# Kernel optimization log

Measured on AMD Instinct MI355X. Metric: run time of the kernel, lower is better.

Reference implementation:

```python
import jax, jax.numpy as jnp
import numpy as np

N_NODES = 50000
N_EDGES = 500000
IN_CH = 128
OUT_CH = 64
HEADS = 4


def setup_inputs() -> dict:
    key = jax.random.key(0)
    ks = jax.random.split(key, 9)
    x = jax.random.normal(ks[0], (N_NODES, IN_CH), dtype=jnp.float32)
    edge_index = jax.random.randint(ks[1], (2, N_EDGES), 0, N_NODES, dtype=jnp.int64)
    edge_weights = jax.random.uniform(ks[2], (N_EDGES, 1), dtype=jnp.float32)
    # xavier-uniform params, stored as [in, out] so y = x @ W
    def xavier(k, shape):
        fan_in, fan_out = shape
        lim = float(np.sqrt(6.0 / (fan_in + fan_out)))
        return jax.random.uniform(k, shape, minval=-lim, maxval=lim, dtype=jnp.float32)
    Wq = xavier(ks[3], (IN_CH, OUT_CH * HEADS))
    Wk = xavier(ks[4], (IN_CH, OUT_CH * HEADS))
    Wv = xavier(ks[5], (IN_CH, OUT_CH * HEADS))
    We = xavier(ks[6], (1, HEADS))
    Wout = xavier(ks[7], (OUT_CH * HEADS, OUT_CH))
    b_out = jnp.zeros((OUT_CH,), dtype=jnp.float32)
    return {"x": x, "edge_index": edge_index, "edge_weights": edge_weights,
            "Wq": Wq, "Wk": Wk, "Wv": Wv, "We": We, "Wout": Wout, "b_out": b_out}


def reference(x, edge_index, edge_weights, Wq, Wk, Wv, We, Wout, b_out):
    num_nodes = x.shape[0]
    src = edge_index[0]
    tgt = edge_index[1]
    x_src = x[src]                                    # [E, in]
    x_tgt = x[tgt]                                    # [E, in]
    q = (x_tgt @ Wq).reshape(-1, HEADS, OUT_CH)       # [E, H, C]
    k = (x_src @ Wk).reshape(-1, HEADS, OUT_CH)
    v = (x_src @ Wv).reshape(-1, HEADS, OUT_CH)
    attn = jnp.sum(q * k, axis=-1) / jnp.sqrt(jnp.float32(OUT_CH))  # [E, H]
    attn = attn + edge_weights @ We                   # [E, H]
    attn = jax.nn.leaky_relu(attn, negative_slope=0.2)
    attn = jax.nn.softmax(attn, axis=0)               # global softmax over edges (as in source)
    weighted_v = attn[..., None] * v                  # [E, H, C]
    out = jax.ops.segment_sum(weighted_v, tgt, num_segments=num_nodes)  # [N, H, C]
    out = out.reshape(num_nodes, HEADS * OUT_CH) @ Wout + b_out         # [N, out]
    if x.shape == out.shape:
        out = out + x
    return out
```

## Files before the change

kernel.cpp:

```cpp
#include <hip/hip_runtime.h>
#include <hip/hip_bf16.h>
#include <hip/hip_fp16.h>

#define N_NODES 50000
#define N_EDGES 500000
#define IN_CH   128
#define D       256
#define UDIM    512
#define OUT_CH  64
#define HEADS   4
#define NC      49

typedef _Float16 half8 __attribute__((ext_vector_type(8)));
typedef _Float16 half2_t __attribute__((ext_vector_type(2)));
typedef float   floatx4 __attribute__((ext_vector_type(4)));

__global__ __launch_bounds__(256) void prep_kernel(const float* __restrict__ x,
                                                   __half* __restrict__ x16,
                                                   int* __restrict__ cnt,
                                                   double* __restrict__ S) {
    int i = blockIdx.x * 256 + threadIdx.x;
    if (i < N_NODES) cnt[i] = 0;
    if (i < HEADS) S[i] = 0.0;
    int k = i * 4;
    if (k < N_NODES * IN_CH) {
        float4 v = *(const float4*)(x + k);
        union { __half2 h[2]; uint2 u; } pk;
        pk.h[0] = __floats2half2_rn(v.x, v.y);
        pk.h[1] = __floats2half2_rn(v.z, v.w);
        *(uint2*)(x16 + k) = pk.u;
    }
}

__global__ __launch_bounds__(128) void wbuild_kernel(const float* __restrict__ Wq,
                                                     const float* __restrict__ Wk,
                                                     const float* __restrict__ Wv,
                                                     const float* __restrict__ Wout,
                                                     __half* __restrict__ M16t,
                                                     __half* __restrict__ Zc16t) {
    __shared__ float buf[64];
    const int tid = threadIdx.x;
    if (blockIdx.x < 512) {
        const int r = blockIdx.x;
        const int h = r >> 7, j = r & 127;
        if (tid < 64) buf[tid] = Wk[(size_t)j * D + h * 64 + tid];
        __syncthreads();
        const float4* qr = (const float4*)(Wq + (size_t)tid * D + h * 64);
        float s = 0.f;
        #pragma unroll
        for (int c4 = 0; c4 < 16; ++c4) {
            float4 q = qr[c4];
            s += q.x * buf[c4 * 4] + q.y * buf[c4 * 4 + 1]
               + q.z * buf[c4 * 4 + 2] + q.w * buf[c4 * 4 + 3];
        }
        M16t[(size_t)r * IN_CH + tid] = __float2half(s);
    } else {
        const int r = blockIdx.x - 512;
        const int h = r >> 7, i = r & 127;
        if (tid < 64) buf[tid] = Wv[(size_t)i * D + h * 64 + tid];
        __syncthreads();
        if (tid < 64) {
            float s = 0.f;
            #pragma unroll 8
            for (int j = 0; j < 64; ++j)
                s += buf[j] * Wout[(size_t)(h * 64 + j) * OUT_CH + tid];
            Zc16t[(size_t)tid * UDIM + r] = __float2half(s);
        }
    }
}

__global__ __launch_bounds__(256) void gemm_u_mfma_kernel(const __half* __restrict__ x16,
                                                          const __half* __restrict__ M16t,
                                                          __half* __restrict__ u16) {
    __shared__ __half Ax[128][136];
    __shared__ __half Bm[128][136];
    const int m0 = blockIdx.x * 128;
    const int colbase = blockIdx.y * 128;
    const int tid = threadIdx.x;

    {
        const int r = tid >> 1, part = tid & 1;
        uint4 va[8];
        if (m0 + r < N_NODES) {
            const uint4* src = (const uint4*)(x16 + (size_t)(m0 + r) * IN_CH + part * 64);
            #pragma unroll
            for (int q = 0; q < 8; ++q) va[q] = src[q];
        } else {
            #pragma unroll
            for (int q = 0; q < 8; ++q) va[q] = make_uint4(0u, 0u, 0u, 0u);
        }
        uint4* da = (uint4*)&Ax[r][part * 64];
        #pragma unroll
        for (int q = 0; q < 8; ++q) da[q] = va[q];
        const uint4* sb = (const uint4*)(M16t + (size_t)(colbase + r) * IN_CH + part * 64);
        uint4* db = (uint4*)&Bm[r][part * 64];
        #pragma unroll
        for (int q = 0; q < 8; ++q) db[q] = sb[q];
    }
    __syncthreads();

    const int w = tid >> 6, lane = tid & 63;
    const int mrow = lane & 15, quad = lane >> 4;

    half8 a[2][4];
    #pragma unroll
    for (int mt = 0; mt < 2; ++mt)
        #pragma unroll
        for (int ks = 0; ks < 4; ++ks)
            a[mt][ks] = *(const half8*)&Ax[w * 32 + mt * 16 + mrow][ks * 32 + quad * 8];

    floatx4 acc[2][8];
    #pragma unroll
    for (int mt = 0; mt < 2; ++mt)
        #pragma unroll
        for (int nt = 0; nt < 8; ++nt)
            acc[mt][nt] = (floatx4){0.f, 0.f, 0.f, 0.f};

    #pragma unroll
    for (int nt = 0; nt < 8; ++nt) {
        #pragma unroll
        for (int ks = 0; ks < 4; ++ks) {
            half8 b = *(const half8*)&Bm[nt * 16 + mrow][ks * 32 + quad * 8];
            acc[0][nt] = __builtin_amdgcn_mfma_f32_16x16x32_f16(a[0][ks], b, acc[0][nt], 0, 0, 0);
            acc[1][nt] = __builtin_amdgcn_mfma_f32_16x16x32_f16(a[1][ks], b, acc[1][nt], 0, 0, 0);
        }
    }
    __syncthreads();
    #pragma unroll
    for (int mt = 0; mt < 2; ++mt)
        #pragma unroll
        for (int nt = 0; nt < 8; ++nt)
            #pragma unroll
            for (int r = 0; r < 4; ++r)
                Ax[w * 32 + mt * 16 + quad * 4 + r][nt * 16 + mrow] = __float2half(acc[mt][nt][r]);
    __syncthreads();
    {
        const int r = tid >> 1, part = tid & 1;
        if (m0 + r < N_NODES) {
            const uint4* s4 = (const uint4*)&Ax[r][part * 64];
            uint4* d4 = (uint4*)(u16 + (size_t)(m0 + r) * UDIM + colbase + part * 64);
            #pragma unroll
            for (int q = 0; q < 8; ++q) d4[q] = s4[q];
        }
    }
}

__global__ __launch_bounds__(256) void hist_kernel(const int* __restrict__ ei,
                                                   int* __restrict__ cnt) {
    int e = blockIdx.x * 256 + threadIdx.x;
    if (e < N_EDGES) atomicAdd(&cnt[ei[N_EDGES + e]], 1);
}

__global__ __launch_bounds__(256) void scan_reduce_kernel(const int* __restrict__ cnt,
                                                          int* __restrict__ csum) {
    const int b = blockIdx.x, tid = threadIdx.x;
    const int lane = tid & 63, wid = tid >> 6;
    int s = 0;
    int idx0 = b * 1024 + tid * 4;
    #pragma unroll
    for (int i = 0; i < 4; ++i) {
        int idx = idx0 + i;
        if (idx < N_NODES) s += cnt[idx];
    }
    #pragma unroll
    for (int m = 1; m < 64; m <<= 1) s += __shfl_xor(s, m, 64);
    __shared__ int w[4];
    if (lane == 0) w[wid] = s;
    __syncthreads();
    if (tid == 0) csum[b] = w[0] + w[1] + w[2] + w[3];
}

__global__ __launch_bounds__(64) void scan_top_kernel(int* __restrict__ csum) {
    int lane = threadIdx.x;
    int v = (lane < NC) ? csum[lane] : 0;
    int x = v;
    #pragma unroll
    for (int d = 1; d < 64; d <<= 1) {
        int y = __shfl_up(x, d, 64);
        if (lane >= d) x += y;
    }
    if (lane < NC) csum[lane] = x - v;
}

__global__ __launch_bounds__(256) void scan_chunks_kernel(int* __restrict__ cnt,
                                                          const int* __restrict__ csum,
                                                          int* __restrict__ rp) {
    const int b = blockIdx.x, tid = threadIdx.x;
    const int lane = tid & 63, wid = tid >> 6;
    __shared__ int wsum[4];
    int v[4];
    const int idx0 = b * 1024 + tid * 4;
    #pragma unroll
    for (int i = 0; i < 4; ++i) {
        int idx = idx0 + i;
        v[i] = (idx < N_NODES) ? cnt[idx] : 0;
    }
    int tsum = v[0] + v[1] + v[2] + v[3];
    int x = tsum;
    #pragma unroll
    for (int d = 1; d < 64; d <<= 1) {
        int y = __shfl_up(x, d, 64);
        if (lane >= d) x += y;
    }
    if (lane == 63) wsum[wid] = x;
    __syncthreads();
    int woff = 0;
    for (int w = 0; w < wid; ++w) woff += wsum[w];
    int excl = csum[b] + woff + x - tsum;
    #pragma unroll
    for (int i = 0; i < 4; ++i) {
        int idx = idx0 + i;
        if (idx < N_NODES) { rp[idx] = excl; cnt[idx] = excl; }
        excl += v[i];
    }
}

__global__ __launch_bounds__(256) void scatter_kernel(const int* __restrict__ ei,
                                                      const float* __restrict__ ew,
                                                      int* __restrict__ cnt,
                                                      int2* __restrict__ payload) {
    int e = blockIdx.x * 256 + threadIdx.x;
    if (e >= N_EDGES) return;
    int s = ei[e], t = ei[N_EDGES + e];
    int pos = atomicAdd(&cnt[t], 1);
    payload[pos] = make_int2(s, __float_as_int(ew[e]));
}

__global__ __launch_bounds__(256) void edge_fused_kernel(const __half* __restrict__ u16,
                                                         const __half* __restrict__ x16,
                                                         const int* __restrict__ rp,
                                                         const int* __restrict__ cnt,
                                                         const int2* __restrict__ payload,
                                                         const float* __restrict__ We,
                                                         __half* __restrict__ y16,
                                                         double* __restrict__ S) {
    const int tid = threadIdx.x;
    const int l16 = tid & 15;
    const int h = l16 >> 2;
    const int q = l16 & 3;
    const int node = blockIdx.x * 16 + (tid >> 4);
    const float wev = We[h];

    uint4 ur[4];
    {
        const uint4* ub = (const uint4*)(u16 + (size_t)node * UDIM + h * 128 + q * 32);
        ur[0] = ub[0]; ur[1] = ub[1]; ur[2] = ub[2]; ur[3] = ub[3];
    }
    const half2_t* uh = (const half2_t*)ur;

    half2_t yacc[16];
    #pragma unroll
    for (int t = 0; t < 16; ++t) yacc[t] = (half2_t){(_Float16)0.f, (_Float16)0.f};

    float sacc = 0.f;
    const int start = rp[node];
    const int end = cnt[node];
    int2 pl = make_int2(0, 0);
    uint4 xr[4];
    if (start < end) {
        pl = payload[start];
        const uint4* xb = (const uint4*)(x16 + (size_t)pl.x * IN_CH + q * 32);
        xr[0] = xb[0]; xr[1] = xb[1]; xr[2] = xb[2]; xr[3] = xb[3];
    }
    for (int e = start; e < end; ++e) {
        int2 pln = pl;
        uint4 xrn[4] = {xr[0], xr[1], xr[2], xr[3]};
        if (e + 1 < end) {
            pln = payload[e + 1];
            const uint4* xb = (const uint4*)(x16 + (size_t)pln.x * IN_CH + q * 32);
            xrn[0] = xb[0]; xrn[1] = xb[1]; xrn[2] = xb[2]; xrn[3] = xb[3];
        }
        const half2_t* xh = (const half2_t*)xr;
        float dot = 0.f;
        #pragma unroll
        for (int t = 0; t < 16; ++t)
            dot = __builtin_amdgcn_fdot2(uh[t], xh[t], dot, false);
        dot += __shfl_xor(dot, 1, 16);
        dot += __shfl_xor(dot, 2, 16);
        float l = dot * 0.125f + __int_as_float(pl.y) * wev;
        l = fmaxf(l, 0.2f * l);
        float p = __expf(l);
        if (q == 0) sacc += p;
        half2_t p2 = (half2_t){(_Float16)p, (_Float16)p};
        #pragma unroll
        for (int t = 0; t < 16; ++t)
            yacc[t] = p2 * xh[t] + yacc[t];
        pl = pln;
        xr[0] = xrn[0]; xr[1] = xrn[1]; xr[2] = xrn[2]; xr[3] = xrn[3];
    }
    {
        uint4* yo = (uint4*)(y16 + (size_t)node * UDIM + h * 128 + q * 32);
        const uint4* ys = (const uint4*)yacc;
        yo[0] = ys[0]; yo[1] = ys[1]; yo[2] = ys[2]; yo[3] = ys[3];
    }
    __shared__ float sblk[4];
    if (tid < 4) sblk[tid] = 0.f;
    __syncthreads();
    if (q == 0) atomicAdd(&sblk[h], sacc);
    __syncthreads();
    if (tid < 4) atomicAdd(&S[tid], (double)sblk[tid]);
}

__global__ __launch_bounds__(256) void gemm_out_mfma_kernel(const __half* __restrict__ y16,
                                                            const __half* __restrict__ Zc16t,
                                                            const double* __restrict__ S,
                                                            const float* __restrict__ b_out,
                                                            float* __restrict__ out) {
    __shared__ __half Ay[128][136];
    __shared__ __half Bz[64][136];
    __shared__ float invs_s[4];
    const int m0 = blockIdx.x * 128;
    const int tid = threadIdx.x;
    if (tid < 4) invs_s[tid] = (float)(1.0 / S[tid]);

    const int w = tid >> 6, lane = tid & 63;
    const int mrow = lane & 15, quad = lane >> 4;

    floatx4 result[2][4];
    #pragma unroll
    for (int mt = 0; mt < 2; ++mt)
        #pragma unroll
        for (int nt = 0; nt < 4; ++nt)
            result[mt][nt] = (floatx4){0.f, 0.f, 0.f, 0.f};

    for (int h = 0; h < HEADS; ++h) {
        {
            const int r = tid >> 1, part = tid & 1;
            uint4 va[8];
            if (m0 + r < N_NODES) {
                const uint4* src = (const uint4*)(y16 + (size_t)(m0 + r) * UDIM + h * 128 + part * 64);
                #pragma unroll
                for (int qq = 0; qq < 8; ++qq) va[qq] = src[qq];
            } else {
                #pragma unroll
                for (int qq = 0; qq < 8; ++qq) va[qq] = make_uint4(0u, 0u, 0u, 0u);
            }
            uint4* da = (uint4*)&Ay[r][part * 64];
            #pragma unroll
            for (int qq = 0; qq < 8; ++qq) da[qq] = va[qq];
        }
        {
            const int r = tid >> 2, part = tid & 3;
            const uint4* sb = (const uint4*)(Zc16t + (size_t)r * UDIM + h * 128 + part * 32);
            uint4* db = (uint4*)&Bz[r][part * 32];
            #pragma unroll
            for (int qq = 0; qq < 4; ++qq) db[qq] = sb[qq];
        }
        __syncthreads();

        half8 a[2][4];
        #pragma unroll
        for (int mt = 0; mt < 2; ++mt)
            #pragma unroll
            for (int ks = 0; ks < 4; ++ks)
                a[mt][ks] = *(const half8*)&Ay[w * 32 + mt * 16 + mrow][ks * 32 + quad * 8];

        floatx4 acc[2][4];
        #pragma unroll
        for (int mt = 0; mt < 2; ++mt)
            #pragma unroll
            for (int nt = 0; nt < 4; ++nt)
                acc[mt][nt] = (floatx4){0.f, 0.f, 0.f, 0.f};

        #pragma unroll
        for (int nt = 0; nt < 4; ++nt) {
            #pragma unroll
            for (int ks = 0; ks < 4; ++ks) {
                half8 b = *(const half8*)&Bz[nt * 16 + mrow][ks * 32 + quad * 8];
                acc[0][nt] = __builtin_amdgcn_mfma_f32_16x16x32_f16(a[0][ks], b, acc[0][nt], 0, 0, 0);
                acc[1][nt] = __builtin_amdgcn_mfma_f32_16x16x32_f16(a[1][ks], b, acc[1][nt], 0, 0, 0);
            }
        }
        const float inv = invs_s[h];
        #pragma unroll
        for (int mt = 0; mt < 2; ++mt)
            #pragma unroll
            for (int nt = 0; nt < 4; ++nt) {
                result[mt][nt][0] += inv * acc[mt][nt][0];
                result[mt][nt][1] += inv * acc[mt][nt][1];
                result[mt][nt][2] += inv * acc[mt][nt][2];
                result[mt][nt][3] += inv * acc[mt][nt][3];
            }
        __syncthreads();
    }
    float bcol[4];
    #pragma unroll
    for (int nt = 0; nt < 4; ++nt) bcol[nt] = b_out[nt * 16 + mrow];
    #pragma unroll
    for (int mt = 0; mt < 2; ++mt) {
        #pragma unroll
        for (int r = 0; r < 4; ++r) {
            int row = m0 + w * 32 + mt * 16 + quad * 4 + r;
            if (row < N_NODES) {
                float* dst = out + (size_t)row * OUT_CH;
                #pragma unroll
                for (int nt = 0; nt < 4; ++nt)
                    dst[nt * 16 + mrow] = result[mt][nt][r] + bcol[nt];
            }
        }
    }
}

extern "C" void kernel_launch(void* const* d_in, const int* in_sizes, int n_in,
                              void* d_out, int out_size, void* d_ws, size_t ws_size,
                              hipStream_t stream) {
    const float* x     = (const float*)d_in[0];
    const int*   ei    = (const int*)d_in[1];
    const float* ew    = (const float*)d_in[2];
    const float* Wq    = (const float*)d_in[3];
    const float* Wk    = (const float*)d_in[4];
    const float* Wv    = (const float*)d_in[5];
    const float* We    = (const float*)d_in[6];
    const float* Wout  = (const float*)d_in[7];
    const float* b_out = (const float*)d_in[8];
    float* out = (float*)d_out;

    __half* u16   = (__half*)d_ws;
    __half* y16   = u16 + (size_t)N_NODES * UDIM;
    __half* x16   = y16 + (size_t)N_NODES * UDIM;
    double* S     = (double*)(x16 + (size_t)N_NODES * IN_CH);
    __half* M16t  = (__half*)(S + HEADS);
    __half* Zc16t = M16t + UDIM * IN_CH;
    int*    rp    = (int*)(Zc16t + OUT_CH * UDIM);
    int*    cnt   = rp + N_NODES;
    int*    csum  = cnt + N_NODES;
    int2*   payload = (int2*)(csum + 64);

    prep_kernel<<<(N_NODES * IN_CH / 4 + 255) / 256, 256, 0, stream>>>(x, x16, cnt, S);
    wbuild_kernel<<<1024, 128, 0, stream>>>(Wq, Wk, Wv, Wout, M16t, Zc16t);
    gemm_u_mfma_kernel<<<dim3((N_NODES + 127) / 128, 4), 256, 0, stream>>>(x16, M16t, u16);
    hist_kernel<<<(N_EDGES + 255) / 256, 256, 0, stream>>>(ei, cnt);
    scan_reduce_kernel<<<NC, 256, 0, stream>>>(cnt, csum);
    scan_top_kernel<<<1, 64, 0, stream>>>(csum);
    scan_chunks_kernel<<<NC, 256, 0, stream>>>(cnt, csum, rp);
    scatter_kernel<<<(N_EDGES + 255) / 256, 256, 0, stream>>>(ei, ew, cnt, payload);
    edge_fused_kernel<<<N_NODES / 16, 256, 0, stream>>>(u16, x16, rp, cnt, payload, We, y16, S);
    gemm_out_mfma_kernel<<<(N_NODES + 127) / 128, 256, 0, stream>>>(y16, Zc16t, S, b_out, out);
}
```

Before: 272.5 us.

## Fuse per-node u projection GEMM into edge kernel via LDS

Removes the standalone gemm_u kernel and computes each block's 16 nodes' 512-wide u vectors with MFMA at the start of the edge kernel, staging them in shared memory. This eliminates writing and re-reading the 50000x512 fp16 u buffer through global memory plus one launch. In exchange each edge block reloads the full M16t matrix from global or cache, the MFMA tiles are only 16 rows so B reuse is low, and LDS use rises, which may reduce occupancy of the latency-bound gather loop.

```diff
diff --git a/kernel.cpp b/kernel.cpp
--- a/kernel.cpp
+++ b/kernel.cpp
@@ -69,82 +69,6 @@
     }
 }
 
-__global__ __launch_bounds__(256) void gemm_u_mfma_kernel(const __half* __restrict__ x16,
-                                                          const __half* __restrict__ M16t,
-                                                          __half* __restrict__ u16) {
-    __shared__ __half Ax[128][136];
-    __shared__ __half Bm[128][136];
-    const int m0 = blockIdx.x * 128;
-    const int colbase = blockIdx.y * 128;
-    const int tid = threadIdx.x;
-
-    {
-        const int r = tid >> 1, part = tid & 1;
-        uint4 va[8];
-        if (m0 + r < N_NODES) {
-            const uint4* src = (const uint4*)(x16 + (size_t)(m0 + r) * IN_CH + part * 64);
-            #pragma unroll
-            for (int q = 0; q < 8; ++q) va[q] = src[q];
-        } else {
-            #pragma unroll
-            for (int q = 0; q < 8; ++q) va[q] = make_uint4(0u, 0u, 0u, 0u);
-        }
-        uint4* da = (uint4*)&Ax[r][part * 64];
-        #pragma unroll
-        for (int q = 0; q < 8; ++q) da[q] = va[q];
-        const uint4* sb = (const uint4*)(M16t + (size_t)(colbase + r) * IN_CH + part * 64);
-        uint4* db = (uint4*)&Bm[r][part * 64];
-        #pragma unroll
-        for (int q = 0; q < 8; ++q) db[q] = sb[q];
-    }
-    __syncthreads();
-
-    const int w = tid >> 6, lane = tid & 63;
-    const int mrow = lane & 15, quad = lane >> 4;
-
-    half8 a[2][4];
-    #pragma unroll
-    for (int mt = 0; mt < 2; ++mt)
-        #pragma unroll
-        for (int ks = 0; ks < 4; ++ks)
-            a[mt][ks] = *(const half8*)&Ax[w * 32 + mt * 16 + mrow][ks * 32 + quad * 8];
-
-    floatx4 acc[2][8];
-    #pragma unroll
-    for (int mt = 0; mt < 2; ++mt)
-        #pragma unroll
-        for (int nt = 0; nt < 8; ++nt)
-            acc[mt][nt] = (floatx4){0.f, 0.f, 0.f, 0.f};
-
-    #pragma unroll
-    for (int nt = 0; nt < 8; ++nt) {
-        #pragma unroll
-        for (int ks = 0; ks < 4; ++ks) {
-            half8 b = *(const half8*)&Bm[nt * 16 + mrow][ks * 32 + quad * 8];
-            acc[0][nt] = __builtin_amdgcn_mfma_f32_16x16x32_f16(a[0][ks], b, acc[0][nt], 0, 0, 0);
-            acc[1][nt] = __builtin_amdgcn_mfma_f32_16x16x32_f16(a[1][ks], b, acc[1][nt], 0, 0, 0);
-        }
-    }
-    __syncthreads();
-    #pragma unroll
-    for (int mt = 0; mt < 2; ++mt)
-        #pragma unroll
-        for (int nt = 0; nt < 8; ++nt)
-            #pragma unroll
-            for (int r = 0; r < 4; ++r)
-                Ax[w * 32 + mt * 16 + quad * 4 + r][nt * 16 + mrow] = __float2half(acc[mt][nt][r]);
-    __syncthreads();
-    {
-        const int r = tid >> 1, part = tid & 1;
-        if (m0 + r < N_NODES) {
-            const uint4* s4 = (const uint4*)&Ax[r][part * 64];
-            uint4* d4 = (uint4*)(u16 + (size_t)(m0 + r) * UDIM + colbase + part * 64);
-            #pragma unroll
-            for (int q = 0; q < 8; ++q) d4[q] = s4[q];
-        }
-    }
-}
-
 __global__ __launch_bounds__(256) void hist_kernel(const int* __restrict__ ei,
                                                    int* __restrict__ cnt) {
     int e = blockIdx.x * 256 + threadIdx.x;
@@ -226,27 +150,53 @@
     payload[pos] = make_int2(s, __float_as_int(ew[e]));
 }
 
-__global__ __launch_bounds__(256) void edge_fused_kernel(const __half* __restrict__ u16,
-                                                         const __half* __restrict__ x16,
+__global__ __launch_bounds__(256) void edge_fused_kernel(const __half* __restrict__ x16,
+                                                         const __half* __restrict__ M16t,
                                                          const int* __restrict__ rp,
                                                          const int* __restrict__ cnt,
                                                          const int2* __restrict__ payload,
                                                          const float* __restrict__ We,
                                                          __half* __restrict__ y16,
                                                          double* __restrict__ S) {
+    __shared__ __half u_lds[16][520];
     const int tid = threadIdx.x;
+    const int nodebase = blockIdx.x * 16;
+
+    {
+        const int w = tid >> 6, lane = tid & 63;
+        const int mrow = lane & 15, quad = lane >> 4;
+        half8 a[4];
+        #pragma unroll
+        for (int ks = 0; ks < 4; ++ks)
+            a[ks] = *(const half8*)(x16 + (size_t)(nodebase + mrow) * IN_CH + ks * 32 + quad * 8);
+        #pragma unroll
+        for (int nt8 = 0; nt8 < 8; ++nt8) {
+            const int nt = w * 8 + nt8;
+            floatx4 acc = (floatx4){0.f, 0.f, 0.f, 0.f};
+            #pragma unroll
+            for (int ks = 0; ks < 4; ++ks) {
+                half8 b = *(const half8*)(M16t + (size_t)(nt * 16 + mrow) * IN_CH + ks * 32 + quad * 8);
+                acc = __builtin_amdgcn_mfma_f32_16x16x32_f16(a[ks], b, acc, 0, 0, 0);
+            }
+            #pragma unroll
+            for (int r = 0; r < 4; ++r)
+                u_lds[quad * 4 + r][nt * 16 + mrow] = __float2half(acc[r]);
+        }
+    }
+    __syncthreads();
+
     const int l16 = tid & 15;
     const int h = l16 >> 2;
     const int q = l16 & 3;
-    const int node = blockIdx.x * 16 + (tid >> 4);
+    const int node = nodebase + (tid >> 4);
     const float wev = We[h];
 
-    uint4 ur[4];
+    uint4 ur4[4];
     {
-        const uint4* ub = (const uint4*)(u16 + (size_t)node * UDIM + h * 128 + q * 32);
-        ur[0] = ub[0]; ur[1] = ub[1]; ur[2] = ub[2]; ur[3] = ub[3];
-    }
-    const half2_t* uh = (const half2_t*)ur;
+        const uint4* ub = (const uint4*)&u_lds[tid >> 4][h * 128 + q * 32];
+        ur4[0] = ub[0]; ur4[1] = ub[1]; ur4[2] = ub[2]; ur4[3] = ub[3];
+    }
+    const half2_t* uh = (const half2_t*)ur4;
 
     half2_t yacc[16];
     #pragma unroll
@@ -415,8 +365,7 @@
     const float* b_out = (const float*)d_in[8];
     float* out = (float*)d_out;
 
-    __half* u16   = (__half*)d_ws;
-    __half* y16   = u16 + (size_t)N_NODES * UDIM;
+    __half* y16   = (__half*)d_ws;
     __half* x16   = y16 + (size_t)N_NODES * UDIM;
     double* S     = (double*)(x16 + (size_t)N_NODES * IN_CH);
     __half* M16t  = (__half*)(S + HEADS);
@@ -428,12 +377,11 @@
 
     prep_kernel<<<(N_NODES * IN_CH / 4 + 255) / 256, 256, 0, stream>>>(x, x16, cnt, S);
     wbuild_kernel<<<1024, 128, 0, stream>>>(Wq, Wk, Wv, Wout, M16t, Zc16t);
-    gemm_u_mfma_kernel<<<dim3((N_NODES + 127) / 128, 4), 256, 0, stream>>>(x16, M16t, u16);
     hist_kernel<<<(N_EDGES + 255) / 256, 256, 0, stream>>>(ei, cnt);
     scan_reduce_kernel<<<NC, 256, 0, stream>>>(cnt, csum);
     scan_top_kernel<<<1, 64, 0, stream>>>(csum);
     scan_chunks_kernel<<<NC, 256, 0, stream>>>(cnt, csum, rp);
     scatter_kernel<<<(N_EDGES + 255) / 256, 256, 0, stream>>>(ei, ew, cnt, payload);
-    edge_fused_kernel<<<N_NODES / 16, 256, 0, stream>>>(u16, x16, rp, cnt, payload, We, y16, S);
+    edge_fused_kernel<<<N_NODES / 16, 256, 0, stream>>>(x16, M16t, rp, cnt, payload, We, y16, S);
     gemm_out_mfma_kernel<<<(N_NODES + 127) / 128, 256, 0, stream>>>(y16, Zc16t, S, b_out, out);
 }
```

Result: slower. 443.6 us (+62.8%).

## Sort nodes by in-degree bucket to balance edge kernel warps

Applied to the files above, without the earlier changes.

Adds a counting sort of nodes by in-degree (histogram, scan, scatter into a permutation), and the fused edge kernel now processes nodes in that order. Nodes that share a wavefront get similar degrees, so lanes spend less time idle while waiting for the longest edge loop. The cost is three extra small kernel launches and an indirection through perm. Adjacent wavefronts also no longer touch contiguous node rows, which hurts locality of the u16 and y16 accesses.

```diff
diff --git a/kernel.cpp b/kernel.cpp
--- a/kernel.cpp
+++ b/kernel.cpp
@@ -10,6 +10,7 @@
 #define OUT_CH  64
 #define HEADS   4
 #define NC      49
+#define DBUCK   128
 
 typedef _Float16 half8 __attribute__((ext_vector_type(8)));
 typedef _Float16 half2_t __attribute__((ext_vector_type(2)));
@@ -18,9 +19,11 @@
 __global__ __launch_bounds__(256) void prep_kernel(const float* __restrict__ x,
                                                    __half* __restrict__ x16,
                                                    int* __restrict__ cnt,
+                                                   int* __restrict__ dcnt,
                                                    double* __restrict__ S) {
     int i = blockIdx.x * 256 + threadIdx.x;
     if (i < N_NODES) cnt[i] = 0;
+    if (i < DBUCK) dcnt[i] = 0;
     if (i < HEADS) S[i] = 0.0;
     int k = i * 4;
     if (k < N_NODES * IN_CH) {
@@ -151,6 +154,38 @@
     if (e < N_EDGES) atomicAdd(&cnt[ei[N_EDGES + e]], 1);
 }
 
+__global__ __launch_bounds__(256) void deghist_kernel(const int* __restrict__ cnt,
+                                                      int* __restrict__ dcnt) {
+    int i = blockIdx.x * 256 + threadIdx.x;
+    if (i < N_NODES) atomicAdd(&dcnt[min(cnt[i], DBUCK - 1)], 1);
+}
+
+__global__ __launch_bounds__(128) void degscan_kernel(int* __restrict__ dcnt) {
+    const int tid = threadIdx.x, lane = tid & 63, wid = tid >> 6;
+    int v = dcnt[tid];
+    int x = v;
+    #pragma unroll
+    for (int d = 1; d < 64; d <<= 1) {
+        int y = __shfl_up(x, d, 64);
+        if (lane >= d) x += y;
+    }
+    __shared__ int w0;
+    if (wid == 0 && lane == 63) w0 = x;
+    __syncthreads();
+    dcnt[tid] = x - v + (wid ? w0 : 0);
+}
+
+__global__ __launch_bounds__(256) void degscatter_kernel(const int* __restrict__ cnt,
+                                                         int* __restrict__ dcnt,
+                                                         int* __restrict__ perm) {
+    int i = blockIdx.x * 256 + threadIdx.x;
+    if (i < N_NODES) {
+        int b = min(cnt[i], DBUCK - 1);
+        int pos = atomicAdd(&dcnt[b], 1);
+        perm[pos] = i;
+    }
+}
+
 __global__ __launch_bounds__(256) void scan_reduce_kernel(const int* __restrict__ cnt,
                                                           int* __restrict__ csum) {
     const int b = blockIdx.x, tid = threadIdx.x;
@@ -228,6 +263,7 @@
 
 __global__ __launch_bounds__(256) void edge_fused_kernel(const __half* __restrict__ u16,
                                                          const __half* __restrict__ x16,
+                                                         const int* __restrict__ perm,
                                                          const int* __restrict__ rp,
                                                          const int* __restrict__ cnt,
                                                          const int2* __restrict__ payload,
@@ -238,15 +274,15 @@
     const int l16 = tid & 15;
     const int h = l16 >> 2;
     const int q = l16 & 3;
-    const int node = blockIdx.x * 16 + (tid >> 4);
+    const int node = perm[blockIdx.x * 16 + (tid >> 4)];
     const float wev = We[h];
 
-    uint4 ur[4];
+    uint4 ur4[4];
     {
         const uint4* ub = (const uint4*)(u16 + (size_t)node * UDIM + h * 128 + q * 32);
-        ur[0] = ub[0]; ur[1] = ub[1]; ur[2] = ub[2]; ur[3] = ub[3];
-    }
-    const half2_t* uh = (const half2_t*)ur;
+        ur4[0] = ub[0]; ur4[1] = ub[1]; ur4[2] = ub[2]; ur4[3] = ub[3];
+    }
+    const half2_t* uh = (const half2_t*)ur4;
 
     half2_t yacc[16];
     #pragma unroll
@@ -424,16 +460,21 @@
     int*    rp    = (int*)(Zc16t + OUT_CH * UDIM);
     int*    cnt   = rp + N_NODES;
     int*    csum  = cnt + N_NODES;
-    int2*   payload = (int2*)(csum + 64);
-
-    prep_kernel<<<(N_NODES * IN_CH / 4 + 255) / 256, 256, 0, stream>>>(x, x16, cnt, S);
+    int*    dcnt  = csum + 64;
+    int*    perm  = dcnt + DBUCK;
+    int2*   payload = (int2*)(perm + N_NODES);
+
+    prep_kernel<<<(N_NODES * IN_CH / 4 + 255) / 256, 256, 0, stream>>>(x, x16, cnt, dcnt, S);
     wbuild_kernel<<<1024, 128, 0, stream>>>(Wq, Wk, Wv, Wout, M16t, Zc16t);
     gemm_u_mfma_kernel<<<dim3((N_NODES + 127) / 128, 4), 256, 0, stream>>>(x16, M16t, u16);
     hist_kernel<<<(N_EDGES + 255) / 256, 256, 0, stream>>>(ei, cnt);
+    deghist_kernel<<<(N_NODES + 255) / 256, 256, 0, stream>>>(cnt, dcnt);
+    degscan_kernel<<<1, 128, 0, stream>>>(dcnt);
+    degscatter_kernel<<<(N_NODES + 255) / 256, 256, 0, stream>>>(cnt, dcnt, perm);
     scan_reduce_kernel<<<NC, 256, 0, stream>>>(cnt, csum);
     scan_top_kernel<<<1, 64, 0, stream>>>(csum);
     scan_chunks_kernel<<<NC, 256, 0, stream>>>(cnt, csum, rp);
     scatter_kernel<<<(N_EDGES + 255) / 256, 256, 0, stream>>>(ei, ew, cnt, payload);
-    edge_fused_kernel<<<N_NODES / 16, 256, 0, stream>>>(u16, x16, rp, cnt, payload, We, y16, S);
+    edge_fused_kernel<<<N_NODES / 16, 256, 0, stream>>>(u16, x16, perm, rp, cnt, payload, We, y16, S);
     gemm_out_mfma_kernel<<<(N_NODES + 127) / 128, 256, 0, stream>>>(y16, Zc16t, S, b_out, out);
 }
```

Result: slower. 589.7 us (+116.4%).

## Merge prep, histogram, weight build and scan stages into fewer launches; stage payload in LDS

Applied to the files above, without the earlier changes.

Cuts the launch count from ten to six: x->fp16 conversion, edge histogram and both weight-product builds now share one kernel, the chunk-sum reduction rides along with the u GEMM, and the top-level scan is computed redundantly inside each scan_chunks block. The cnt zeroing moves to a memset. The edge kernel also stages each block's contiguous payload span into shared memory, falling back to global memory past a 1024-entry cap. The aim is to remove launch gaps and small serial kernels, at the cost of mixed-role blocks and extra LDS use in the edge kernel.

```diff
diff --git a/kernel.cpp b/kernel.cpp
--- a/kernel.cpp
+++ b/kernel.cpp
@@ -10,42 +10,53 @@
 #define OUT_CH  64
 #define HEADS   4
 #define NC      49
+#define PCAP    1024
+
+#define NB_X16  6250
+#define NB_HIST 1954
+#define NB_MB   256
+#define NB_ZB   128
+#define NB_GEMM 1564
 
 typedef _Float16 half8 __attribute__((ext_vector_type(8)));
 typedef _Float16 half2_t __attribute__((ext_vector_type(2)));
 typedef float   floatx4 __attribute__((ext_vector_type(4)));
 
-__global__ __launch_bounds__(256) void prep_kernel(const float* __restrict__ x,
-                                                   __half* __restrict__ x16,
-                                                   int* __restrict__ cnt,
-                                                   double* __restrict__ S) {
-    int i = blockIdx.x * 256 + threadIdx.x;
-    if (i < N_NODES) cnt[i] = 0;
-    if (i < HEADS) S[i] = 0.0;
-    int k = i * 4;
-    if (k < N_NODES * IN_CH) {
-        float4 v = *(const float4*)(x + k);
-        union { __half2 h[2]; uint2 u; } pk;
-        pk.h[0] = __floats2half2_rn(v.x, v.y);
-        pk.h[1] = __floats2half2_rn(v.z, v.w);
-        *(uint2*)(x16 + k) = pk.u;
-    }
-}
-
-__global__ __launch_bounds__(128) void wbuild_kernel(const float* __restrict__ Wq,
-                                                     const float* __restrict__ Wk,
-                                                     const float* __restrict__ Wv,
-                                                     const float* __restrict__ Wout,
-                                                     __half* __restrict__ M16t,
-                                                     __half* __restrict__ Zc16t) {
-    __shared__ float buf[64];
-    const int tid = threadIdx.x;
-    if (blockIdx.x < 512) {
-        const int r = blockIdx.x;
+__global__ __launch_bounds__(256) void k1_prep_kernel(const float* __restrict__ x,
+                                                      __half* __restrict__ x16,
+                                                      const int* __restrict__ ei,
+                                                      int* __restrict__ cnt,
+                                                      double* __restrict__ S,
+                                                      const float* __restrict__ Wq,
+                                                      const float* __restrict__ Wk,
+                                                      const float* __restrict__ Wv,
+                                                      const float* __restrict__ Wout,
+                                                      __half* __restrict__ M16t,
+                                                      __half* __restrict__ Zc16t) {
+    __shared__ float sbuf[4][64];
+    const int b = blockIdx.x, tid = threadIdx.x;
+    if (b < NB_X16) {
+        int i = b * 256 + tid;
+        if (i < HEADS) S[i] = 0.0;
+        int k = i * 4;
+        if (k < N_NODES * IN_CH) {
+            float4 v = *(const float4*)(x + k);
+            union { __half2 h[2]; uint2 u; } pk;
+            pk.h[0] = __floats2half2_rn(v.x, v.y);
+            pk.h[1] = __floats2half2_rn(v.z, v.w);
+            *(uint2*)(x16 + k) = pk.u;
+        }
+    } else if (b < NB_X16 + NB_HIST) {
+        int e = (b - NB_X16) * 256 + tid;
+        if (e < N_EDGES) atomicAdd(&cnt[ei[N_EDGES + e]], 1);
+    } else if (b < NB_X16 + NB_HIST + NB_MB) {
+        const int r = (b - NB_X16 - NB_HIST) * 2 + (tid >> 7);
+        const int i = tid & 127;
         const int h = r >> 7, j = r & 127;
-        if (tid < 64) buf[tid] = Wk[(size_t)j * D + h * 64 + tid];
+        float* buf = sbuf[tid >> 7];
+        if (i < 64) buf[i] = Wk[(size_t)j * D + h * 64 + i];
         __syncthreads();
-        const float4* qr = (const float4*)(Wq + (size_t)tid * D + h * 64);
+        const float4* qr = (const float4*)(Wq + (size_t)i * D + h * 64);
         float s = 0.f;
         #pragma unroll
         for (int c4 = 0; c4 < 16; ++c4) {
@@ -53,31 +64,50 @@
             s += q.x * buf[c4 * 4] + q.y * buf[c4 * 4 + 1]
                + q.z * buf[c4 * 4 + 2] + q.w * buf[c4 * 4 + 3];
         }
-        M16t[(size_t)r * IN_CH + tid] = __float2half(s);
+        M16t[(size_t)r * IN_CH + i] = __float2half(s);
     } else {
-        const int r = blockIdx.x - 512;
+        const int r = (b - NB_X16 - NB_HIST - NB_MB) * 4 + (tid >> 6);
+        const int c = tid & 63;
         const int h = r >> 7, i = r & 127;
-        if (tid < 64) buf[tid] = Wv[(size_t)i * D + h * 64 + tid];
+        float* buf = sbuf[tid >> 6];
+        buf[c] = Wv[(size_t)i * D + h * 64 + c];
         __syncthreads();
-        if (tid < 64) {
-            float s = 0.f;
-            #pragma unroll 8
-            for (int j = 0; j < 64; ++j)
-                s += buf[j] * Wout[(size_t)(h * 64 + j) * OUT_CH + tid];
-            Zc16t[(size_t)tid * UDIM + r] = __float2half(s);
-        }
-    }
-}
-
-__global__ __launch_bounds__(256) void gemm_u_mfma_kernel(const __half* __restrict__ x16,
-                                                          const __half* __restrict__ M16t,
-                                                          __half* __restrict__ u16) {
+        float s = 0.f;
+        #pragma unroll 8
+        for (int j = 0; j < 64; ++j)
+            s += buf[j] * Wout[(size_t)(h * 64 + j) * OUT_CH + c];
+        Zc16t[(size_t)c * UDIM + r] = __float2half(s);
+    }
+}
+
+__global__ __launch_bounds__(256) void k2_gemmu_kernel(const __half* __restrict__ x16,
+                                                       const __half* __restrict__ M16t,
+                                                       __half* __restrict__ u16,
+                                                       const int* __restrict__ cnt,
+                                                       int* __restrict__ csum) {
     __shared__ __half Ax[128][136];
     __shared__ __half Bm[128][136];
-    const int m0 = blockIdx.x * 128;
-    const int colbase = blockIdx.y * 128;
     const int tid = threadIdx.x;
-
+    if (blockIdx.x >= NB_GEMM) {
+        const int b = blockIdx.x - NB_GEMM;
+        const int lane = tid & 63, wid = tid >> 6;
+        int s = 0;
+        int idx0 = b * 1024 + tid * 4;
+        #pragma unroll
+        for (int i = 0; i < 4; ++i) {
+            int idx = idx0 + i;
+            if (idx < N_NODES) s += cnt[idx];
+        }
+        #pragma unroll
+        for (int m = 1; m < 64; m <<= 1) s += __shfl_xor(s, m, 64);
+        int* w4 = (int*)Ax;
+        if (lane == 0) w4[wid] = s;
+        __syncthreads();
+        if (tid == 0) csum[b] = w4[0] + w4[1] + w4[2] + w4[3];
+        return;
+    }
+    const int m0 = (blockIdx.x % 391) * 128;
+    const int colbase = (blockIdx.x / 391) * 128;
     {
         const int r = tid >> 1, part = tid & 1;
         uint4 va[8];
@@ -120,9 +150,9 @@
     for (int nt = 0; nt < 8; ++nt) {
         #pragma unroll
         for (int ks = 0; ks < 4; ++ks) {
-            half8 b = *(const half8*)&Bm[nt * 16 + mrow][ks * 32 + quad * 8];
-            acc[0][nt] = __builtin_amdgcn_mfma_f32_16x16x32_f16(a[0][ks], b, acc[0][nt], 0, 0, 0);
-            acc[1][nt] = __builtin_amdgcn_mfma_f32_16x16x32_f16(a[1][ks], b, acc[1][nt], 0, 0, 0);
+            half8 bfr = *(const half8*)&Bm[nt * 16 + mrow][ks * 32 + quad * 8];
+            acc[0][nt] = __builtin_amdgcn_mfma_f32_16x16x32_f16(a[0][ks], bfr, acc[0][nt], 0, 0, 0);
+            acc[1][nt] = __builtin_amdgcn_mfma_f32_16x16x32_f16(a[1][ks], bfr, acc[1][nt], 0, 0, 0);
         }
     }
     __syncthreads();
@@ -145,68 +175,36 @@
     }
 }
 
-__global__ __launch_bounds__(256) void hist_kernel(const int* __restrict__ ei,
-                                                   int* __restrict__ cnt) {
-    int e = blockIdx.x * 256 + threadIdx.x;
-    if (e < N_EDGES) atomicAdd(&cnt[ei[N_EDGES + e]], 1);
-}
-
-__global__ __launch_bounds__(256) void scan_reduce_kernel(const int* __restrict__ cnt,
-                                                          int* __restrict__ csum) {
+__global__ __launch_bounds__(256) void k3_scan_chunks_kernel(int* __restrict__ cnt,
+                                                             const int* __restrict__ csum,
+                                                             int* __restrict__ rp) {
+    __shared__ int stop[64];
+    __shared__ int wsum[4];
     const int b = blockIdx.x, tid = threadIdx.x;
     const int lane = tid & 63, wid = tid >> 6;
-    int s = 0;
-    int idx0 = b * 1024 + tid * 4;
+    if (tid < 64) stop[tid] = (tid < NC) ? csum[tid] : 0;
+    __syncthreads();
+    int base = 0;
+    for (int w = 0; w < b; ++w) base += stop[w];
+    int v[4];
+    const int idx0 = b * 1024 + tid * 4;
     #pragma unroll
     for (int i = 0; i < 4; ++i) {
         int idx = idx0 + i;
-        if (idx < N_NODES) s += cnt[idx];
-    }
-    #pragma unroll
-    for (int m = 1; m < 64; m <<= 1) s += __shfl_xor(s, m, 64);
-    __shared__ int w[4];
-    if (lane == 0) w[wid] = s;
-    __syncthreads();
-    if (tid == 0) csum[b] = w[0] + w[1] + w[2] + w[3];
-}
-
-__global__ __launch_bounds__(64) void scan_top_kernel(int* __restrict__ csum) {
-    int lane = threadIdx.x;
-    int v = (lane < NC) ? csum[lane] : 0;
-    int x = v;
+        v[i] = (idx < N_NODES) ? cnt[idx] : 0;
+    }
+    int tsum = v[0] + v[1] + v[2] + v[3];
+    int x = tsum;
     #pragma unroll
     for (int d = 1; d < 64; d <<= 1) {
         int y = __shfl_up(x, d, 64);
         if (lane >= d) x += y;
     }
-    if (lane < NC) csum[lane] = x - v;
-}
-
-__global__ __launch_bounds__(256) void scan_chunks_kernel(int* __restrict__ cnt,
-                                                          const int* __restrict__ csum,
-                                                          int* __restrict__ rp) {
-    const int b = blockIdx.x, tid = threadIdx.x;
-    const int lane = tid & 63, wid = tid >> 6;
-    __shared__ int wsum[4];
-    int v[4];
-    const int idx0 = b * 1024 + tid * 4;
-    #pragma unroll
-    for (int i = 0; i < 4; ++i) {
-        int idx = idx0 + i;
-        v[i] = (idx < N_NODES) ? cnt[idx] : 0;
-    }
-    int tsum = v[0] + v[1] + v[2] + v[3];
-    int x = tsum;
-    #pragma unroll
-    for (int d = 1; d < 64; d <<= 1) {
-        int y = __shfl_up(x, d, 64);
-        if (lane >= d) x += y;
-    }
     if (lane == 63) wsum[wid] = x;
     __syncthreads();
     int woff = 0;
     for (int w = 0; w < wid; ++w) woff += wsum[w];
-    int excl = csum[b] + woff + x - tsum;
+    int excl = base + woff + x - tsum;
     #pragma unroll
     for (int i = 0; i < 4; ++i) {
         int idx = idx0 + i;
@@ -234,19 +232,30 @@
                                                          const float* __restrict__ We,
                                                          __half* __restrict__ y16,
                                                          double* __restrict__ S) {
+    __shared__ int2 pbuf[PCAP];
+    __shared__ float sblk[4];
     const int tid = threadIdx.x;
+    const int nodebase = blockIdx.x * 16;
+
+    const int span0 = rp[nodebase];
+    const int span1 = cnt[nodebase + 15];
+    const int span_len = min(span1 - span0, PCAP);
+    for (int i = tid; i < span_len; i += 256) pbuf[i] = payload[span0 + i];
+    if (tid < 4) sblk[tid] = 0.f;
+    __syncthreads();
+
     const int l16 = tid & 15;
     const int h = l16 >> 2;
     const int q = l16 & 3;
-    const int node = blockIdx.x * 16 + (tid >> 4);
+    const int node = nodebase + (tid >> 4);
     const float wev = We[h];
 
-    uint4 ur[4];
+    uint4 ur4[4];
     {
         const uint4* ub = (const uint4*)(u16 + (size_t)node * UDIM + h * 128 + q * 32);
-        ur[0] = ub[0]; ur[1] = ub[1]; ur[2] = ub[2]; ur[3] = ub[3];
-    }
-    const half2_t* uh = (const half2_t*)ur;
+        ur4[0] = ub[0]; ur4[1] = ub[1]; ur4[2] = ub[2]; ur4[3] = ub[3];
+    }
+    const half2_t* uh = (const half2_t*)ur4;
 
     half2_t yacc[16];
     #pragma unroll
@@ -255,10 +264,16 @@
     float sacc = 0.f;
     const int start = rp[node];
     const int end = cnt[node];
+
+    auto getpl = [&](int e) -> int2 {
+        int idx = e - span0;
+        return (idx < PCAP) ? pbuf[idx] : payload[e];
+    };
+
     int2 pl = make_int2(0, 0);
     uint4 xr[4];
     if (start < end) {
-        pl = payload[start];
+        pl = getpl(start);
         const uint4* xb = (const uint4*)(x16 + (size_t)pl.x * IN_CH + q * 32);
         xr[0] = xb[0]; xr[1] = xb[1]; xr[2] = xb[2]; xr[3] = xb[3];
     }
@@ -266,7 +281,7 @@
         int2 pln = pl;
         uint4 xrn[4] = {xr[0], xr[1], xr[2], xr[3]};
         if (e + 1 < end) {
-            pln = payload[e + 1];
+            pln = getpl(e + 1);
             const uint4* xb = (const uint4*)(x16 + (size_t)pln.x * IN_CH + q * 32);
             xrn[0] = xb[0]; xrn[1] = xb[1]; xrn[2] = xb[2]; xrn[3] = xb[3];
         }
@@ -293,8 +308,6 @@
         const uint4* ys = (const uint4*)yacc;
         yo[0] = ys[0]; yo[1] = ys[1]; yo[2] = ys[2]; yo[3] = ys[3];
     }
-    __shared__ float sblk[4];
-    if (tid < 4) sblk[tid] = 0.f;
     __syncthreads();
     if (q == 0) atomicAdd(&sblk[h], sacc);
     __syncthreads();
@@ -366,9 +379,9 @@
         for (int nt = 0; nt < 4; ++nt) {
             #pragma unroll
             for (int ks = 0; ks < 4; ++ks) {
-                half8 b = *(const half8*)&Bz[nt * 16 + mrow][ks * 32 + quad * 8];
-                acc[0][nt] = __builtin_amdgcn_mfma_f32_16x16x32_f16(a[0][ks], b, acc[0][nt], 0, 0, 0);
-                acc[1][nt] = __builtin_amdgcn_mfma_f32_16x16x32_f16(a[1][ks], b, acc[1][nt], 0, 0, 0);
+                half8 bfr = *(const half8*)&Bz[nt * 16 + mrow][ks * 32 + quad * 8];
+                acc[0][nt] = __builtin_amdgcn_mfma_f32_16x16x32_f16(a[0][ks], bfr, acc[0][nt], 0, 0, 0);
+                acc[1][nt] = __builtin_amdgcn_mfma_f32_16x16x32_f16(a[1][ks], bfr, acc[1][nt], 0, 0, 0);
             }
         }
         const float inv = invs_s[h];
@@ -426,13 +439,11 @@
     int*    csum  = cnt + N_NODES;
     int2*   payload = (int2*)(csum + 64);
 
-    prep_kernel<<<(N_NODES * IN_CH / 4 + 255) / 256, 256, 0, stream>>>(x, x16, cnt, S);
-    wbuild_kernel<<<1024, 128, 0, stream>>>(Wq, Wk, Wv, Wout, M16t, Zc16t);
-    gemm_u_mfma_kernel<<<dim3((N_NODES + 127) / 128, 4), 256, 0, stream>>>(x16, M16t, u16);
-    hist_kernel<<<(N_EDGES + 255) / 256, 256, 0, stream>>>(ei, cnt);
-    scan_reduce_kernel<<<NC, 256, 0, stream>>>(cnt, csum);
-    scan_top_kernel<<<1, 64, 0, stream>>>(csum);
-    scan_chunks_kernel<<<NC, 256, 0, stream>>>(cnt, csum, rp);
+    hipMemsetAsync(cnt, 0, N_NODES * sizeof(int), stream);
+    k1_prep_kernel<<<NB_X16 + NB_HIST + NB_MB + NB_ZB, 256, 0, stream>>>(
+        x, x16, ei, cnt, S, Wq, Wk, Wv, Wout, M16t, Zc16t);
+    k2_gemmu_kernel<<<NB_GEMM + NC, 256, 0, stream>>>(x16, M16t, u16, cnt, csum);
+    k3_scan_chunks_kernel<<<NC, 256, 0, stream>>>(cnt, csum, rp);
     scatter_kernel<<<(N_EDGES + 255) / 256, 256, 0, stream>>>(ei, ew, cnt, payload);
     edge_fused_kernel<<<N_NODES / 16, 256, 0, stream>>>(u16, x16, rp, cnt, payload, We, y16, S);
     gemm_out_mfma_kernel<<<(N_NODES + 127) / 128, 256, 0, stream>>>(y16, Zc16t, S, b_out, out);
```

Measured after the change: 263.1 us. 1.04x faster.
